# Performance work log

Hardware: AMD Instinct MI355X
Metric: run time of the kernel (lower is better)

## Reference

```python
import jax, jax.numpy as jnp
import numpy as np

E = 1024      # embed_dim
H = 16        # num_heads
HD = E // H   # head_dim = 64


def setup_inputs() -> dict:
    key = jax.random.key(0)
    ks = jax.random.split(key, 8)
    T, B, S = 1024, 4, 1024
    return {
        "query": jax.random.normal(ks[0], (T, B, E), jnp.float32),
        "key": jax.random.normal(ks[1], (S, B, E), jnp.float32),
        "value": jax.random.normal(ks[2], (S, B, E), jnp.float32),
        "attn_mask": jax.random.normal(ks[3], (T, S), jnp.float32),
        "key_padding_mask": jax.random.randint(ks[4], (B, S), 0, 2, jnp.int32),
        "in_proj_weight": jax.random.normal(ks[5], (3 * E, E), jnp.float32) * 0.02,
        "in_proj_bias": jnp.zeros((3 * E,), jnp.float32),
        "out_w": jax.random.normal(ks[6], (E, E), jnp.float32) * 0.02,
        "out_b": jnp.zeros((E,), jnp.float32),
    }


def reference(query, key, value, attn_mask, key_padding_mask,
              in_proj_weight, in_proj_bias, out_w, out_b):
    T, B, _ = query.shape
    S = key.shape[0]
    w_q, w_k, w_v = jnp.split(in_proj_weight, 3, axis=0)   # each [E, E]
    b_q, b_k, b_v = jnp.split(in_proj_bias, 3, axis=0)
    q = query @ w_q.T + b_q                                # [T, B, E]
    k = key @ w_k.T + b_k                                  # [S, B, E]
    v = value @ w_v.T + b_v                                # [S, B, E]
    # [len, B, E] -> [B*H, len, HD]
    q = q.reshape(T, B * H, HD).transpose(1, 0, 2) / jnp.sqrt(jnp.float32(HD))
    k = k.reshape(S, B * H, HD).transpose(1, 0, 2)
    v = v.reshape(S, B * H, HD).transpose(1, 0, 2)
    scores = jnp.einsum('bth,bsh->bts', q, k)              # [B*H, T, S]
    scores = scores + attn_mask[None]                      # float additive mask
    pad = key_padding_mask.astype(bool)                    # [B, S]
    pad = jnp.broadcast_to(pad[:, None, None, :], (B, H, 1, S)).reshape(B * H, 1, S)
    scores = jnp.where(pad, -jnp.inf, scores)
    weights = jax.nn.softmax(scores, axis=-1)              # dropout p=0 -> identity
    out = jnp.einsum('bts,bsh->bth', weights, v)           # [B*H, T, HD]
    out = out.transpose(1, 0, 2).reshape(T, B, E)
    out = out @ out_w.T + out_b
    weights_avg = weights.reshape(B, H, T, S).mean(axis=1) # sum/H == mean
    return out, weights_avg
```

## Files before the change

kernel.cpp:

```cpp
#include <hip/hip_runtime.h>
#include <stdint.h>

typedef short bf16x8 __attribute__((ext_vector_type(8)));
typedef float f32x4  __attribute__((ext_vector_type(4)));

#define LOG2E_F 1.4426950408889634f
#define QSCALE_F 0.1803368801111204f

__device__ __forceinline__ unsigned short f2bf(float f) {
    unsigned int u = __float_as_uint(f);
    return (unsigned short)((u + 0x7FFFu + ((u >> 16) & 1u)) >> 16);
}

__device__ __forceinline__ unsigned short f2bfu(float f) {
    return (unsigned short)((__float_as_uint(f) + 0x8000u) >> 16);
}

__device__ __forceinline__ uint4 pack8(float4 a, float4 b) {
    union { unsigned short us[8]; uint4 v; } p;
    p.us[0] = f2bf(a.x); p.us[1] = f2bf(a.y); p.us[2] = f2bf(a.z); p.us[3] = f2bf(a.w);
    p.us[4] = f2bf(b.x); p.us[5] = f2bf(b.y); p.us[6] = f2bf(b.z); p.us[7] = f2bf(b.w);
    return p.v;
}

__device__ __forceinline__ void gload_lds16(const unsigned short* g, unsigned short* l) {
    __builtin_amdgcn_global_load_lds(
        (const __attribute__((address_space(1))) void*)g,
        (__attribute__((address_space(3))) void*)l, 16, 0, 0);
}

__global__ __launch_bounds__(256)
void cvt_kernel(const float* __restrict__ q, const float* __restrict__ k,
                const float* __restrict__ v, const float* __restrict__ w,
                const float* __restrict__ ow,
                uint4* __restrict__ Xb, uint4* __restrict__ Wb, uint4* __restrict__ OWb)
{
    const unsigned g = blockIdx.x * 256 + threadIdx.x;
    const float* src;
    uint4* dst;
    if (g < 1572864u) {
        dst = Xb + g;
        if (g < 524288u)        src = q + (size_t)g * 8;
        else if (g < 1048576u)  src = k + (size_t)(g - 524288u) * 8;
        else                    src = v + (size_t)(g - 1048576u) * 8;
    } else if (g < 1966080u) {
        src = w + (size_t)(g - 1572864u) * 8;
        dst = Wb + (g - 1572864u);
    } else {
        src = ow + (size_t)(g - 1966080u) * 8;
        dst = OWb + (g - 1966080u);
    }
    float4 a = *(const float4*)src;
    float4 b = *(const float4*)(src + 4);
    *dst = pack8(a, b);
}

__global__ __launch_bounds__(256)
void mtr_kernel(const float* __restrict__ m, float* __restrict__ mt)
{
    __shared__ float tile[64][65];
    const int bt = (blockIdx.x & 15) << 6;
    const int bs = (blockIdx.x >> 4) << 6;
    const int tx = threadIdx.x & 63;
    const int ty = threadIdx.x >> 6;
#pragma unroll
    for (int i = 0; i < 64; i += 4)
        tile[ty + i][tx] = m[(size_t)(bt + ty + i) * 1024 + bs + tx];
    __syncthreads();
#pragma unroll
    for (int i = 0; i < 64; i += 4) {
        const int s = bs + ty + i;
        mt[(size_t)(s >> 2) * 4096 + (bt + tx) * 4 + (s & 3)] = tile[tx][ty + i];
    }
}

__global__ __launch_bounds__(256)
void qkv_proj_kernel(const unsigned short* __restrict__ Xb, const unsigned short* __restrict__ Wb,
                     const float* __restrict__ bias,
                     unsigned short* __restrict__ Qb, unsigned short* __restrict__ Kb,
                     unsigned short* __restrict__ Vtb)
{
    const int z = blockIdx.z;
    const int j   = blockIdx.x;
    const int xcd = j & 7, idx = j >> 3;
    const int row0 = ((xcd << 2) + (idx >> 3)) * 128;
    const int col0 = (idx & 7) * 128;
    const int wofs = z << 10;

    const unsigned short* A = Xb + (size_t)z * 4194304;
    const unsigned short* B = Wb;

    __shared__ __align__(16) unsigned short As[128 * 32];
    __shared__ __align__(16) unsigned short Bs[128 * 32];

    const int tid  = threadIdx.x;
    const int lane = tid & 63;
    const int wv   = tid >> 6;
    const int wr   = wv >> 1, wc = wv & 1;
    const int c16  = lane & 15;
    const int kof  = (lane >> 4) << 3;

    const f32x4 zero4 = {0.f, 0.f, 0.f, 0.f};
    f32x4 acc[4][4];
#pragma unroll
    for (int m = 0; m < 4; ++m)
#pragma unroll
        for (int n = 0; n < 4; ++n) acc[m][n] = zero4;

    const unsigned short* gA = A + (size_t)(row0 + wv * 16 + (lane >> 2)) * 1024 + ((lane & 3) << 3);
    const unsigned short* gB = B + (size_t)(wofs + col0 + wv * 16 + (lane >> 2)) * 1024 + ((lane & 3) << 3);
    unsigned short* lA = As + tid * 8;
    unsigned short* lB = Bs + tid * 8;

    const int arow = wr * 64 + c16;
    const int brow = wc * 64 + c16;

    for (int k0 = 0; k0 < 1024; k0 += 32) {
        __syncthreads();
        gload_lds16(gA + k0,         lA);
        gload_lds16(gA + k0 + 65536, lA + 2048);
        gload_lds16(gB + k0,         lB);
        gload_lds16(gB + k0 + 65536, lB + 2048);
        __syncthreads();

        bf16x8 af[4], bfr[4];
#pragma unroll
        for (int m = 0; m < 4; ++m)
            af[m] = *(const bf16x8*)&As[(arow + m * 16) * 32 + kof];
#pragma unroll
        for (int n = 0; n < 4; ++n)
            bfr[n] = *(const bf16x8*)&Bs[(brow + n * 16) * 32 + kof];
#pragma unroll
        for (int m = 0; m < 4; ++m)
#pragma unroll
            for (int n = 0; n < 4; ++n)
                acc[m][n] = __builtin_amdgcn_mfma_f32_16x16x32_bf16(af[m], bfr[n], acc[m][n], 0, 0, 0);
    }

    const int ccol = c16;
    const int crow = (lane >> 4) << 2;
#pragma unroll
    for (int n = 0; n < 4; ++n) {
        const int gc   = col0 + wc * 64 + n * 16 + ccol;
        const float bv = bias[wofs + gc];
        const int head = gc >> 6, d = gc & 63;
#pragma unroll
        for (int m = 0; m < 4; ++m) {
#pragma unroll
            for (int r = 0; r < 4; ++r) {
                const int gr = row0 + wr * 64 + m * 16 + crow + r;
                const int t  = gr >> 2, b = gr & 3;
                const int bh = (b << 4) + head;
                float vv = acc[m][n][r] + bv;
                if (z == 0)      Qb [((size_t)bh << 16) + ((size_t)t << 6) + d]  = f2bf(vv * QSCALE_F);
                else if (z == 1) Kb [((size_t)bh << 16) + ((size_t)t << 6) + d]  = f2bf(vv);
                else             Vtb[((size_t)bh << 16) + ((size_t)d << 10) + t] = f2bf(vv);
            }
        }
    }
}

__global__ __launch_bounds__(512)
void flash_kernel(const unsigned short* __restrict__ Qb, const unsigned short* __restrict__ Kb,
                  const unsigned short* __restrict__ Vtb, const float* __restrict__ maskT,
                  const int* __restrict__ padmask,
                  float* __restrict__ rl_buf, unsigned short* __restrict__ attn_out)
{
    const int j   = blockIdx.x;
    const int xcd = j & 7, idx = j >> 3;
    const int bh  = xcd * 8 + (idx >> 3);
    const int t0  = (idx & 7) << 7;
    const int b   = bh >> 4, h = bh & 15;

    __shared__ __align__(16) unsigned short Ks[2][2][64 * 72];
    __shared__ __align__(16) unsigned short Vs[2][2][64 * 72];

    const int tid  = threadIdx.x;
    const int lane = tid & 63;
    const int wv   = tid >> 6;
    const int kof  = (lane >> 4) << 3;
    const int c16  = lane & 15;
    const int g4   = (lane >> 4) << 2;

    const unsigned short* Qbase = Qb  + ((size_t)bh << 16);
    const unsigned short* Kbase = Kb  + ((size_t)bh << 16);
    const unsigned short* Vbase = Vtb + ((size_t)bh << 16);

    bf16x8 qf[2];
#pragma unroll
    for (int kk = 0; kk < 2; ++kk)
        qf[kk] = *(const bf16x8*)(Qbase + ((size_t)(t0 + wv * 16 + c16) << 6) + kk * 32 + kof);

    const bf16x8 ones = {16256, 16256, 16256, 16256, 16256, 16256, 16256, 16256};

    const f32x4 zero4 = {0.f, 0.f, 0.f, 0.f};
    f32x4 acco[4];
#pragma unroll
    for (int nd = 0; nd < 4; ++nd) acco[nd] = zero4;
    f32x4 acc_l = zero4;

    const int srow_st = tid >> 3;
    const int scol_st = (tid & 7) << 3;

    const int bb  = scol_st & 31;
    const int hh  = scol_st & 32;
    const int cL  = hh + ((bb & 15) >> 2) * 8 + (bb >> 4) * 4;
    const int bb4 = bb + 4;
    const int cH  = hh + ((bb4 & 15) >> 2) * 8 + (bb4 >> 4) * 4;

    const int tr2 = t0 + wv * 16 + c16;

    const unsigned short* kp = Kbase + ((size_t)srow_st << 6) + scol_st;
    const unsigned short* vp = Vbase + ((size_t)srow_st << 10) + scol_st;
    uint4 kA = *(const uint4*)kp;
    uint4 kB = *(const uint4*)(kp + 4096);
    uint4 vA = *(const uint4*)vp;
    uint4 vB = *(const uint4*)(vp + 64);

    {
        *(uint4*)&Ks[0][0][srow_st * 72 + scol_st] = kA;
        *(uint4*)&Ks[0][1][srow_st * 72 + scol_st] = kB;
        uint2 lo, hi;
        lo.x = vA.x; lo.y = vA.y; hi.x = vA.z; hi.y = vA.w;
        *(uint2*)&Vs[0][0][srow_st * 72 + cL] = lo;
        *(uint2*)&Vs[0][0][srow_st * 72 + cH] = hi;
        lo.x = vB.x; lo.y = vB.y; hi.x = vB.z; hi.y = vB.w;
        *(uint2*)&Vs[0][1][srow_st * 72 + cL] = lo;
        *(uint2*)&Vs[0][1][srow_st * 72 + cH] = hi;
    }
    kp = Kbase + ((size_t)(128 + srow_st) << 6) + scol_st;
    vp = Vbase + ((size_t)srow_st << 10) + 128 + scol_st;
    kA = *(const uint4*)kp;
    kB = *(const uint4*)(kp + 4096);
    vA = *(const uint4*)vp;
    vB = *(const uint4*)(vp + 64);
    __syncthreads();

    for (int rd = 0; rd < 8; ++rd) {
        const int cur = rd & 1;
        const int s0  = rd << 7;

        if (rd < 7) {
            *(uint4*)&Ks[cur ^ 1][0][srow_st * 72 + scol_st] = kA;
            *(uint4*)&Ks[cur ^ 1][1][srow_st * 72 + scol_st] = kB;
            uint2 lo, hi;
            lo.x = vA.x; lo.y = vA.y; hi.x = vA.z; hi.y = vA.w;
            *(uint2*)&Vs[cur ^ 1][0][srow_st * 72 + cL] = lo;
            *(uint2*)&Vs[cur ^ 1][0][srow_st * 72 + cH] = hi;
            lo.x = vB.x; lo.y = vB.y; hi.x = vB.z; hi.y = vB.w;
            *(uint2*)&Vs[cur ^ 1][1][srow_st * 72 + cL] = lo;
            *(uint2*)&Vs[cur ^ 1][1][srow_st * 72 + cH] = hi;
        }
        if (rd < 6) {
            const int sn = s0 + 256;
            kp = Kbase + ((size_t)(sn + srow_st) << 6) + scol_st;
            vp = Vbase + ((size_t)srow_st << 10) + sn + scol_st;
            kA = *(const uint4*)kp;
            kB = *(const uint4*)(kp + 4096);
            vA = *(const uint4*)vp;
            vB = *(const uint4*)(vp + 64);
        }

        f32x4 accsA[4], accsB[4];
#pragma unroll
        for (int n = 0; n < 4; ++n) { accsA[n] = zero4; accsB[n] = zero4; }
        __builtin_amdgcn_s_setprio(1);
#pragma unroll
        for (int n = 0; n < 4; ++n) {
            bf16x8 kfA0 = *(const bf16x8*)&Ks[cur][0][(n * 16 + c16) * 72 + kof];
            bf16x8 kfA1 = *(const bf16x8*)&Ks[cur][0][(n * 16 + c16) * 72 + 32 + kof];
            accsA[n] = __builtin_amdgcn_mfma_f32_16x16x32_bf16(kfA0, qf[0], accsA[n], 0, 0, 0);
            accsA[n] = __builtin_amdgcn_mfma_f32_16x16x32_bf16(kfA1, qf[1], accsA[n], 0, 0, 0);
            bf16x8 kfB0 = *(const bf16x8*)&Ks[cur][1][(n * 16 + c16) * 72 + kof];
            bf16x8 kfB1 = *(const bf16x8*)&Ks[cur][1][(n * 16 + c16) * 72 + 32 + kof];
            accsB[n] = __builtin_amdgcn_mfma_f32_16x16x32_bf16(kfB0, qf[0], accsB[n], 0, 0, 0);
            accsB[n] = __builtin_amdgcn_mfma_f32_16x16x32_bf16(kfB1, qf[1], accsB[n], 0, 0, 0);
        }
        __builtin_amdgcn_s_setprio(0);

#pragma unroll
        for (int tile = 0; tile < 2; ++tile) {
            const int s0t = s0 + tile * 64;
            f32x4* accs = tile ? accsB : accsA;

            float4 mk[4];
            int4 pd[4];
#pragma unroll
            for (int n = 0; n < 4; ++n) {
                const int srow = s0t + n * 16 + g4;
                pd[n] = *(const int4*)(padmask + (b << 10) + srow);
                mk[n] = *(const float4*)(maskT + (size_t)(srow >> 2) * 4096 + tr2 * 4);
            }

            union { unsigned short us[16]; bf16x8 v[2]; } pk;
#pragma unroll
            for (int n = 0; n < 4; ++n) {
                float x0 = fmaf(mk[n].x, LOG2E_F, accs[n][0]);
                float x1 = fmaf(mk[n].y, LOG2E_F, accs[n][1]);
                float x2 = fmaf(mk[n].z, LOG2E_F, accs[n][2]);
                float x3 = fmaf(mk[n].w, LOG2E_F, accs[n][3]);
                if (pd[n].x) x0 = -1e30f;
                if (pd[n].y) x1 = -1e30f;
                if (pd[n].z) x2 = -1e30f;
                if (pd[n].w) x3 = -1e30f;
                pk.us[n * 4 + 0] = f2bfu(__builtin_amdgcn_exp2f(x0));
                pk.us[n * 4 + 1] = f2bfu(__builtin_amdgcn_exp2f(x1));
                pk.us[n * 4 + 2] = f2bfu(__builtin_amdgcn_exp2f(x2));
                pk.us[n * 4 + 3] = f2bfu(__builtin_amdgcn_exp2f(x3));
            }

            __builtin_amdgcn_s_setprio(1);
#pragma unroll
            for (int hhh = 0; hhh < 2; ++hhh) {
                bf16x8 pf = pk.v[hhh];
#pragma unroll
                for (int nd = 0; nd < 4; ++nd) {
                    bf16x8 vf = *(const bf16x8*)&Vs[cur][tile][(nd * 16 + c16) * 72 + hhh * 32 + kof];
                    acco[nd] = __builtin_amdgcn_mfma_f32_16x16x32_bf16(pf, vf, acco[nd], 0, 0, 0);
                }
                acc_l = __builtin_amdgcn_mfma_f32_16x16x32_bf16(pf, ones, acc_l, 0, 0, 0);
            }
            __builtin_amdgcn_s_setprio(0);
        }

        if (rd < 7) __syncthreads();
    }

#pragma unroll
    for (int r = 0; r < 4; ++r) {
        const int t = t0 + wv * 16 + g4 + r;
        const float rl = 1.0f / acc_l[r];
        if (c16 == 0)
            rl_buf[(bh << 10) + t] = rl;
#pragma unroll
        for (int nd = 0; nd < 4; ++nd) {
            const int d = nd * 16 + c16;
            attn_out[((size_t)t * 4 + b) * 1024 + h * 64 + d] = f2bf(acco[nd][r] * rl);
        }
    }
}

__global__ __launch_bounds__(256)
void wavg_kernel(const unsigned short* __restrict__ Qb, const unsigned short* __restrict__ Kb,
                 const float* __restrict__ attn_mask, const int* __restrict__ padmask,
                 const float* __restrict__ rl_buf, float* __restrict__ wout)
{
    const int j   = blockIdx.x;
    const int xcd = j & 7;
    const int b   = xcd >> 1;
    const int rr  = ((j >> 3) << 1) + (xcd & 1);
    const int t0  = (rr >> 4) << 6;
    const int s0  = (rr & 15) << 6;

    __shared__ __align__(16) unsigned short Qs[2][64 * 72];
    __shared__ __align__(16) unsigned short Ks2[2][64 * 72];

    const int tid  = threadIdx.x;
    const int lane = tid & 63;
    const int wv   = tid >> 6;
    const int wr   = wv >> 1, wc = wv & 1;
    const int kof  = (lane >> 4) << 3;
    const int srow_st = tid >> 2;
    const int scol_st = (tid & 3) << 4;

    const int t_base = t0 + wr * 32 + ((lane >> 4) << 2);
    const int s_base = s0 + wc * 32 + (lane & 15);

    int pad2[2];
#pragma unroll
    for (int nn = 0; nn < 2; ++nn) pad2[nn] = padmask[(b << 10) + s_base + nn * 16];

    float maskv[2][2][4];
#pragma unroll
    for (int mm = 0; mm < 2; ++mm)
#pragma unroll
        for (int r = 0; r < 4; ++r)
#pragma unroll
            for (int nn = 0; nn < 2; ++nn)
                maskv[mm][nn][r] = attn_mask[(size_t)(t_base + mm * 16 + r) * 1024 + s_base + nn * 16] * LOG2E_F;

    float wsum[2][2][4];
#pragma unroll
    for (int mm = 0; mm < 2; ++mm)
#pragma unroll
        for (int nn = 0; nn < 2; ++nn)
#pragma unroll
            for (int r = 0; r < 4; ++r) wsum[mm][nn][r] = 0.f;

    const unsigned short* qsrc = Qb + ((size_t)(t0 + srow_st) << 6) + scol_st;
    const unsigned short* ksrc = Kb + ((size_t)(s0 + srow_st) << 6) + scol_st;
    const size_t bh0 = (size_t)(b << 4) << 16;

    uint4 q0 = *(const uint4*)(qsrc + bh0);
    uint4 q1 = *(const uint4*)(qsrc + bh0 + 8);
    uint4 k0 = *(const uint4*)(ksrc + bh0);
    uint4 k1 = *(const uint4*)(ksrc + bh0 + 8);
    *(uint4*)&Qs[0][srow_st * 72 + scol_st]      = q0;
    *(uint4*)&Qs[0][srow_st * 72 + scol_st + 8]  = q1;
    *(uint4*)&Ks2[0][srow_st * 72 + scol_st]     = k0;
    *(uint4*)&Ks2[0][srow_st * 72 + scol_st + 8] = k1;
    q0 = *(const uint4*)(qsrc + bh0 + 65536);
    q1 = *(const uint4*)(qsrc + bh0 + 65536 + 8);
    k0 = *(const uint4*)(ksrc + bh0 + 65536);
    k1 = *(const uint4*)(ksrc + bh0 + 65536 + 8);
    __syncthreads();

#pragma unroll 2
    for (int h = 0; h < 16; ++h) {
        const int cur = h & 1;
        const int bh  = (b << 4) + h;

        if (h < 15) {
            *(uint4*)&Qs[cur ^ 1][srow_st * 72 + scol_st]      = q0;
            *(uint4*)&Qs[cur ^ 1][srow_st * 72 + scol_st + 8]  = q1;
            *(uint4*)&Ks2[cur ^ 1][srow_st * 72 + scol_st]     = k0;
            *(uint4*)&Ks2[cur ^ 1][srow_st * 72 + scol_st + 8] = k1;
        }
        if (h < 14) {
            const size_t of = bh0 + (size_t)(h + 2) * 65536;
            q0 = *(const uint4*)(qsrc + of);
            q1 = *(const uint4*)(qsrc + of + 8);
            k0 = *(const uint4*)(ksrc + of);
            k1 = *(const uint4*)(ksrc + of + 8);
        }

        float rlv[2][4];
#pragma unroll
        for (int mm = 0; mm < 2; ++mm)
#pragma unroll
            for (int r = 0; r < 4; ++r)
                rlv[mm][r] = rl_buf[(bh << 10) + t_base + mm * 16 + r];

        const f32x4 zero4 = {0.f, 0.f, 0.f, 0.f};
        f32x4 accs[2][2];
#pragma unroll
        for (int mm = 0; mm < 2; ++mm)
#pragma unroll
            for (int nn = 0; nn < 2; ++nn) accs[mm][nn] = zero4;
#pragma unroll
        for (int nn = 0; nn < 2; ++nn) {
            bf16x8 kf0 = *(const bf16x8*)&Ks2[cur][(wc * 32 + nn * 16 + (lane & 15)) * 72 + kof];
            bf16x8 kf1 = *(const bf16x8*)&Ks2[cur][(wc * 32 + nn * 16 + (lane & 15)) * 72 + 32 + kof];
#pragma unroll
            for (int mm = 0; mm < 2; ++mm) {
                bf16x8 qf0 = *(const bf16x8*)&Qs[cur][(wr * 32 + mm * 16 + (lane & 15)) * 72 + kof];
                bf16x8 qf1 = *(const bf16x8*)&Qs[cur][(wr * 32 + mm * 16 + (lane & 15)) * 72 + 32 + kof];
                accs[mm][nn] = __builtin_amdgcn_mfma_f32_16x16x32_bf16(qf0, kf0, accs[mm][nn], 0, 0, 0);
                accs[mm][nn] = __builtin_amdgcn_mfma_f32_16x16x32_bf16(qf1, kf1, accs[mm][nn], 0, 0, 0);
            }
        }
#pragma unroll
        for (int mm = 0; mm < 2; ++mm)
#pragma unroll
            for (int nn = 0; nn < 2; ++nn)
#pragma unroll
                for (int r = 0; r < 4; ++r)
                    if (!pad2[nn]) {
                        float x = accs[mm][nn][r] + maskv[mm][nn][r];
                        wsum[mm][nn][r] += __builtin_amdgcn_exp2f(x) * rlv[mm][r];
                    }

        if (h < 15) __syncthreads();
    }

#pragma unroll
    for (int mm = 0; mm < 2; ++mm)
#pragma unroll
        for (int nn = 0; nn < 2; ++nn)
#pragma unroll
            for (int r = 0; r < 4; ++r)
                wout[((size_t)b << 20) + (size_t)(t_base + mm * 16 + r) * 1024 + s_base + nn * 16]
                    = wsum[mm][nn][r] * 0.0625f;
}

__global__ __launch_bounds__(256)
void out_proj_kernel(const unsigned short* __restrict__ A, const unsigned short* __restrict__ Wb,
                     const float* __restrict__ bias, float* __restrict__ out)
{
    const int j   = blockIdx.x;
    const int xcd = j & 7, idx = j >> 3;
    const int row0 = ((xcd << 2) + (idx >> 3)) * 128;
    const int col0 = (idx & 7) * 128;

    __shared__ __align__(16) unsigned short As[128 * 32];
    __shared__ __align__(16) unsigned short Bs[128 * 32];

    const int tid  = threadIdx.x;
    const int lane = tid & 63;
    const int wv   = tid >> 6;
    const int wr   = wv >> 1, wc = wv & 1;
    const int c16  = lane & 15;
    const int kof  = (lane >> 4) << 3;

    const f32x4 zero4 = {0.f, 0.f, 0.f, 0.f};
    f32x4 acc[4][4];
#pragma unroll
    for (int m = 0; m < 4; ++m)
#pragma unroll
        for (int n = 0; n < 4; ++n) acc[m][n] = zero4;

    const unsigned short* gA = A  + (size_t)(row0 + wv * 16 + (lane >> 2)) * 1024 + ((lane & 3) << 3);
    const unsigned short* gB = Wb + (size_t)(col0 + wv * 16 + (lane >> 2)) * 1024 + ((lane & 3) << 3);
    unsigned short* lA = As + tid * 8;
    unsigned short* lB = Bs + tid * 8;

    const int arow = wr * 64 + c16;
    const int brow = wc * 64 + c16;

    for (int k0 = 0; k0 < 1024; k0 += 32) {
        __syncthreads();
        gload_lds16(gA + k0,         lA);
        gload_lds16(gA + k0 + 65536, lA + 2048);
        gload_lds16(gB + k0,         lB);
        gload_lds16(gB + k0 + 65536, lB + 2048);
        __syncthreads();

        bf16x8 af[4], bfr[4];
#pragma unroll
        for (int m = 0; m < 4; ++m)
            af[m] = *(const bf16x8*)&As[(arow + m * 16) * 32 + kof];
#pragma unroll
        for (int n = 0; n < 4; ++n)
            bfr[n] = *(const bf16x8*)&Bs[(brow + n * 16) * 32 + kof];
#pragma unroll
        for (int m = 0; m < 4; ++m)
#pragma unroll
            for (int n = 0; n < 4; ++n)
                acc[m][n] = __builtin_amdgcn_mfma_f32_16x16x32_bf16(af[m], bfr[n], acc[m][n], 0, 0, 0);
    }

    const int ccol = c16;
    const int crow = (lane >> 4) << 2;
#pragma unroll
    for (int n = 0; n < 4; ++n) {
        const int gc   = col0 + wc * 64 + n * 16 + ccol;
        const float bv = bias[gc];
#pragma unroll
        for (int m = 0; m < 4; ++m) {
#pragma unroll
            for (int r = 0; r < 4; ++r) {
                const int gr = row0 + wr * 64 + m * 16 + crow + r;
                out[(size_t)gr * 1024 + gc] = acc[m][n][r] + bv;
            }
        }
    }
}

extern "C" void kernel_launch(void* const* d_in, const int* in_sizes, int n_in,
                              void* d_out, int out_size, void* d_ws, size_t ws_size,
                              hipStream_t stream)
{
    const float* query     = (const float*)d_in[0];
    const float* key       = (const float*)d_in[1];
    const float* value     = (const float*)d_in[2];
    const float* attn_mask = (const float*)d_in[3];
    const int*   padmask   = (const int*)  d_in[4];
    const float* in_proj_w = (const float*)d_in[5];
    const float* in_proj_b = (const float*)d_in[6];
    const float* out_w     = (const float*)d_in[7];
    const float* out_b     = (const float*)d_in[8];

    float* out  = (float*)d_out;
    float* wavg = out + 4194304;

    char* ws = (char*)d_ws;
    unsigned short* Qb     = (unsigned short*)(ws);
    unsigned short* Kb     = (unsigned short*)(ws + 8388608);
    unsigned short* Vtb    = (unsigned short*)(ws + 16777216);
    unsigned short* Xb     = (unsigned short*)(ws + 25165824);
    unsigned short* attn_o = (unsigned short*)(ws + 25165824);
    float*          maskT  = (float*)(ws + 33554432);
    unsigned short* Wb     = (unsigned short*)(ws + 50331648);
    unsigned short* OWb    = (unsigned short*)(ws + 56623104);
    float*          rl_buf = (float*)(ws + 58720256);

    cvt_kernel<<<dim3(8192), 256, 0, stream>>>(query, key, value, in_proj_w, out_w,
                                               (uint4*)Xb, (uint4*)Wb, (uint4*)OWb);
    qkv_proj_kernel<<<dim3(256, 1, 3), 256, 0, stream>>>(Xb, Wb, in_proj_b, Qb, Kb, Vtb);
    mtr_kernel<<<dim3(256), 256, 0, stream>>>(attn_mask, maskT);
    flash_kernel<<<dim3(512), 512, 0, stream>>>(Qb, Kb, Vtb, maskT, padmask,
                                                rl_buf, attn_o);
    wavg_kernel<<<dim3(1024), 256, 0, stream>>>(Qb, Kb, attn_mask, padmask,
                                                rl_buf, wavg);
    out_proj_kernel<<<dim3(256), 256, 0, stream>>>(attn_o, OWb, out_b, out);
}
```

Measured before the change: 154.0 us.

## Pre-swizzle V layout in projection and load K/V tiles via direct global-to-LDS

The projection kernel now writes V in a pre-permuted, XOR-swizzled tile layout that matches the flash kernel's LDS read pattern, and K is fetched with an XOR swizzle on the global side. The flash kernel replaces register-staged K/V loads and scattered LDS stores with global_load_lds direct copies into unpadded, swizzled shared buffers. This is meant to remove the register round-trip and the padding-based bank-conflict avoidance, which frees registers and LDS. It depends on the swizzle being correct and on async LDS loads completing before the barrier.

```diff
diff --git a/kernel.cpp b/kernel.cpp
--- a/kernel.cpp
+++ b/kernel.cpp
@@ -27,6 +27,13 @@
     __builtin_amdgcn_global_load_lds(
         (const __attribute__((address_space(1))) void*)g,
         (__attribute__((address_space(3))) void*)l, 16, 0, 0);
+}
+
+__device__ __forceinline__ int tauinv(int x) {
+    const int j4 = x & 7, hh = x & 32, bb = x & 24;
+    if (j4 < 4) return hh + ((bb & 15) >> 2) * 8 + (bb >> 4) * 4 + j4;
+    const int b2 = bb + 4;
+    return hh + ((b2 & 15) >> 2) * 8 + (b2 >> 4) * 4 + (j4 - 4);
 }
 
 __global__ __launch_bounds__(256)
@@ -146,15 +153,28 @@
         const int head = gc >> 6, d = gc & 63;
 #pragma unroll
         for (int m = 0; m < 4; ++m) {
-#pragma unroll
-            for (int r = 0; r < 4; ++r) {
-                const int gr = row0 + wr * 64 + m * 16 + crow + r;
-                const int t  = gr >> 2, b = gr & 3;
-                const int bh = (b << 4) + head;
-                float vv = acc[m][n][r] + bv;
-                if (z == 0)      Qb [((size_t)bh << 16) + ((size_t)t << 6) + d]  = f2bf(vv * QSCALE_F);
-                else if (z == 1) Kb [((size_t)bh << 16) + ((size_t)t << 6) + d]  = f2bf(vv);
-                else             Vtb[((size_t)bh << 16) + ((size_t)d << 10) + t] = f2bf(vv);
+            const int tt = (row0 + wr * 64 + m * 16 + crow) >> 2;
+            if (z == 2) {
+                const int R     = tt >> 7;
+                const int tileb = (tt >> 6) & 1;
+                const int col   = tauinv(tt & 63);
+                const int lc    = tileb * 8 + (col >> 3);
+                const int jj    = col & 7;
+                const int pc    = lc ^ (d & 7);
+                const size_t of = ((size_t)(d) << 7) + (pc << 3) + jj;
+#pragma unroll
+                for (int r = 0; r < 4; ++r) {
+                    const int bh = (r << 4) + head;
+                    Vtb[(((size_t)bh * 8 + R) << 13) + of] = f2bf(acc[m][n][r] + bv);
+                }
+            } else {
+#pragma unroll
+                for (int r = 0; r < 4; ++r) {
+                    const int bh = (r << 4) + head;
+                    const float vv = acc[m][n][r] + bv;
+                    if (z == 0) Qb[((size_t)bh << 16) + ((size_t)tt << 6) + d] = f2bf(vv * QSCALE_F);
+                    else        Kb[((size_t)bh << 16) + ((size_t)tt << 6) + d] = f2bf(vv);
+                }
             }
         }
     }
@@ -172,19 +192,20 @@
     const int t0  = (idx & 7) << 7;
     const int b   = bh >> 4, h = bh & 15;
 
-    __shared__ __align__(16) unsigned short Ks[2][2][64 * 72];
-    __shared__ __align__(16) unsigned short Vs[2][2][64 * 72];
+    __shared__ __align__(16) unsigned short Ks[2][2][64 * 64];
+    __shared__ __align__(16) unsigned short Vs[2][64 * 128];
 
     const int tid  = threadIdx.x;
     const int lane = tid & 63;
     const int wv   = tid >> 6;
     const int kof  = (lane >> 4) << 3;
+    const int gq   = lane >> 4;
     const int c16  = lane & 15;
-    const int g4   = (lane >> 4) << 2;
+    const int g4   = gq << 2;
 
     const unsigned short* Qbase = Qb  + ((size_t)bh << 16);
     const unsigned short* Kbase = Kb  + ((size_t)bh << 16);
-    const unsigned short* Vbase = Vtb + ((size_t)bh << 16);
+    const unsigned short* Vsig  = Vtb + ((size_t)bh << 16);
 
     bf16x8 qf[2];
 #pragma unroll
@@ -199,41 +220,21 @@
     for (int nd = 0; nd < 4; ++nd) acco[nd] = zero4;
     f32x4 acc_l = zero4;
 
-    const int srow_st = tid >> 3;
-    const int scol_st = (tid & 7) << 3;
-
-    const int bb  = scol_st & 31;
-    const int hh  = scol_st & 32;
-    const int cL  = hh + ((bb & 15) >> 2) * 8 + (bb >> 4) * 4;
-    const int bb4 = bb + 4;
-    const int cH  = hh + ((bb4 & 15) >> 2) * 8 + (bb4 >> 4) * 4;
+    const int strow = tid >> 3;
+    const unsigned short* gK = Kbase + ((size_t)strow << 6) + (((tid & 7) ^ (strow & 7)) << 3);
+    unsigned short* lK0a = &Ks[0][0][tid * 8];
+    unsigned short* lK0b = &Ks[0][1][tid * 8];
+    unsigned short* lK1a = &Ks[1][0][tid * 8];
+    unsigned short* lK1b = &Ks[1][1][tid * 8];
+    unsigned short* lV0  = &Vs[0][tid * 8];
+    unsigned short* lV1  = &Vs[1][tid * 8];
 
     const int tr2 = t0 + wv * 16 + c16;
 
-    const unsigned short* kp = Kbase + ((size_t)srow_st << 6) + scol_st;
-    const unsigned short* vp = Vbase + ((size_t)srow_st << 10) + scol_st;
-    uint4 kA = *(const uint4*)kp;
-    uint4 kB = *(const uint4*)(kp + 4096);
-    uint4 vA = *(const uint4*)vp;
-    uint4 vB = *(const uint4*)(vp + 64);
-
-    {
-        *(uint4*)&Ks[0][0][srow_st * 72 + scol_st] = kA;
-        *(uint4*)&Ks[0][1][srow_st * 72 + scol_st] = kB;
-        uint2 lo, hi;
-        lo.x = vA.x; lo.y = vA.y; hi.x = vA.z; hi.y = vA.w;
-        *(uint2*)&Vs[0][0][srow_st * 72 + cL] = lo;
-        *(uint2*)&Vs[0][0][srow_st * 72 + cH] = hi;
-        lo.x = vB.x; lo.y = vB.y; hi.x = vB.z; hi.y = vB.w;
-        *(uint2*)&Vs[0][1][srow_st * 72 + cL] = lo;
-        *(uint2*)&Vs[0][1][srow_st * 72 + cH] = hi;
-    }
-    kp = Kbase + ((size_t)(128 + srow_st) << 6) + scol_st;
-    vp = Vbase + ((size_t)srow_st << 10) + 128 + scol_st;
-    kA = *(const uint4*)kp;
-    kB = *(const uint4*)(kp + 4096);
-    vA = *(const uint4*)vp;
-    vB = *(const uint4*)(vp + 64);
+    gload_lds16(gK,        lK0a);
+    gload_lds16(gK + 4096, lK0b);
+    gload_lds16(Vsig + tid * 8,        lV0);
+    gload_lds16(Vsig + 4096 + tid * 8, lV0 + 4096);
     __syncthreads();
 
     for (int rd = 0; rd < 8; ++rd) {
@@ -241,24 +242,12 @@
         const int s0  = rd << 7;
 
         if (rd < 7) {
-            *(uint4*)&Ks[cur ^ 1][0][srow_st * 72 + scol_st] = kA;
-            *(uint4*)&Ks[cur ^ 1][1][srow_st * 72 + scol_st] = kB;
-            uint2 lo, hi;
-            lo.x = vA.x; lo.y = vA.y; hi.x = vA.z; hi.y = vA.w;
-            *(uint2*)&Vs[cur ^ 1][0][srow_st * 72 + cL] = lo;
-            *(uint2*)&Vs[cur ^ 1][0][srow_st * 72 + cH] = hi;
-            lo.x = vB.x; lo.y = vB.y; hi.x = vB.z; hi.y = vB.w;
-            *(uint2*)&Vs[cur ^ 1][1][srow_st * 72 + cL] = lo;
-            *(uint2*)&Vs[cur ^ 1][1][srow_st * 72 + cH] = hi;
-        }
-        if (rd < 6) {
-            const int sn = s0 + 256;
-            kp = Kbase + ((size_t)(sn + srow_st) << 6) + scol_st;
-            vp = Vbase + ((size_t)srow_st << 10) + sn + scol_st;
-            kA = *(const uint4*)kp;
-            kB = *(const uint4*)(kp + 4096);
-            vA = *(const uint4*)vp;
-            vB = *(const uint4*)(vp + 64);
+            const size_t kofs = (size_t)(s0 + 128) << 6;
+            gload_lds16(gK + kofs,        cur ? lK0a : lK1a);
+            gload_lds16(gK + kofs + 4096, cur ? lK0b : lK1b);
+            const size_t vofs = (size_t)(rd + 1) << 13;
+            gload_lds16(Vsig + vofs + tid * 8,        cur ? lV0 : lV1);
+            gload_lds16(Vsig + vofs + 4096 + tid * 8, (cur ? lV0 : lV1) + 4096);
         }
 
         f32x4 accsA[4], accsB[4];
@@ -267,12 +256,16 @@
         __builtin_amdgcn_s_setprio(1);
 #pragma unroll
         for (int n = 0; n < 4; ++n) {
-            bf16x8 kfA0 = *(const bf16x8*)&Ks[cur][0][(n * 16 + c16) * 72 + kof];
-            bf16x8 kfA1 = *(const bf16x8*)&Ks[cur][0][(n * 16 + c16) * 72 + 32 + kof];
+            const int rowK = n * 16 + c16;
+            const int swzK = rowK & 7;
+            const int o0 = rowK * 64 + ((gq ^ swzK) << 3);
+            const int o1 = rowK * 64 + (((4 + gq) ^ swzK) << 3);
+            bf16x8 kfA0 = *(const bf16x8*)&Ks[cur][0][o0];
+            bf16x8 kfA1 = *(const bf16x8*)&Ks[cur][0][o1];
             accsA[n] = __builtin_amdgcn_mfma_f32_16x16x32_bf16(kfA0, qf[0], accsA[n], 0, 0, 0);
             accsA[n] = __builtin_amdgcn_mfma_f32_16x16x32_bf16(kfA1, qf[1], accsA[n], 0, 0, 0);
-            bf16x8 kfB0 = *(const bf16x8*)&Ks[cur][1][(n * 16 + c16) * 72 + kof];
-            bf16x8 kfB1 = *(const bf16x8*)&Ks[cur][1][(n * 16 + c16) * 72 + 32 + kof];
+            bf16x8 kfB0 = *(const bf16x8*)&Ks[cur][1][o0];
+            bf16x8 kfB1 = *(const bf16x8*)&Ks[cur][1][o1];
             accsB[n] = __builtin_amdgcn_mfma_f32_16x16x32_bf16(kfB0, qf[0], accsB[n], 0, 0, 0);
             accsB[n] = __builtin_amdgcn_mfma_f32_16x16x32_bf16(kfB1, qf[1], accsB[n], 0, 0, 0);
         }
@@ -313,9 +306,11 @@
 #pragma unroll
             for (int hhh = 0; hhh < 2; ++hhh) {
                 bf16x8 pf = pk.v[hhh];
+                const int lc = tile * 8 + hhh * 4 + gq;
 #pragma unroll
                 for (int nd = 0; nd < 4; ++nd) {
-                    bf16x8 vf = *(const bf16x8*)&Vs[cur][tile][(nd * 16 + c16) * 72 + hhh * 32 + kof];
+                    const int rowV = nd * 16 + c16;
+                    bf16x8 vf = *(const bf16x8*)&Vs[cur][rowV * 128 + ((lc ^ (rowV & 7)) << 3)];
                     acco[nd] = __builtin_amdgcn_mfma_f32_16x16x32_bf16(pf, vf, acco[nd], 0, 0, 0);
                 }
                 acc_l = __builtin_amdgcn_mfma_f32_16x16x32_bf16(pf, ones, acc_l, 0, 0, 0);
```

After: 140.2 us. -8.9%, faster.
